# Optimization experiments

Hardware: AMD Instinct MI355X
Metric: run time of the kernel (lower is better)

## Reference

```python
import jax, jax.numpy as jnp
import numpy as np

N = 500_000   # active voxels
K = 27        # 3x3x3 kernel offsets
CIN = 32
COUT = 64
EPS = 1e-5


def setup_inputs() -> dict:
    key = jax.random.key(0)
    ks = jax.random.split(key, 9)
    x_feats = jax.random.normal(ks[0], (N, CIN), jnp.float32)
    # neighbor map: for each kernel offset k and output voxel i, index of the
    # input voxel contributing through offset k (submanifold conv, stride=1)
    nbr = jax.random.randint(ks[1], (K, N), 0, N, jnp.int32)
    s1 = 1.0 / np.sqrt(K * CIN)
    s2 = 1.0 / np.sqrt(K * COUT)
    w1 = jax.random.normal(ks[2], (K, CIN, COUT), jnp.float32) * s1
    w2 = jax.random.normal(ks[3], (K, COUT, COUT), jnp.float32) * s2
    g1 = jnp.ones((COUT,), jnp.float32)
    b1 = jnp.zeros((COUT,), jnp.float32)
    g2 = jnp.ones((COUT,), jnp.float32)
    b2 = jnp.zeros((COUT,), jnp.float32)
    wid = jax.random.normal(ks[4], (CIN, COUT), jnp.float32) * (1.0 / np.sqrt(CIN))
    gid = jnp.ones((COUT,), jnp.float32)
    bid = jnp.zeros((COUT,), jnp.float32)
    return {"x_feats": x_feats, "nbr": nbr, "w1": w1, "g1": g1, "b1": b1,
            "w2": w2, "g2": g2, "b2": b2, "wid": wid, "gid": gid, "bid": bid}


def _sparse_conv(feats, nbr, W):
    # feats [N, Cin], nbr [K, N], W [K, Cin, Cout]
    # scan over the fixed 27 kernel offsets: gather -> matmul -> accumulate
    def step(acc, kw):
        idx, w = kw
        return acc + feats[idx] @ w, None
    out0 = jnp.zeros((feats.shape[0], W.shape[-1]), feats.dtype)
    out, _ = jax.lax.scan(step, out0, (nbr, W))
    return out


def _bn(x, g, b):
    # training-mode BatchNorm1d over the voxel axis (biased variance, as torch)
    m = jnp.mean(x, axis=0)
    v = jnp.var(x, axis=0)
    return (x - m) * jax.lax.rsqrt(v + EPS) * g + b


def reference(x_feats, nbr, w1, g1, b1, w2, g2, b2, wid, gid, bid):
    h = jax.nn.relu(_bn(_sparse_conv(x_feats, nbr, w1), g1, b1))
    h = _bn(_sparse_conv(h, nbr, w2), g2, b2)
    ident = _bn(x_feats @ wid, gid, bid)
    return jax.nn.relu(h + ident)
```

## Files before the change

kernel.cpp:

```cpp
#include <hip/hip_runtime.h>

#define NV 500000
#define KOFF 27
#define CIN_ 32
#define COUT_ 64
#define EPS_ 1e-5f

typedef __attribute__((ext_vector_type(8))) _Float16 half8;
typedef __attribute__((ext_vector_type(4))) float floatx4;


__global__ void zero_stats_kernel(float* __restrict__ s) {
  if (threadIdx.x < 384) s[threadIdx.x] = 0.f;
}

__global__ __launch_bounds__(256) void cast_x_kernel(
    const float* __restrict__ x, _Float16* __restrict__ xh) {
  size_t q = (size_t)blockIdx.x * 256 + threadIdx.x;
  if (q >= (size_t)NV * CIN_ / 8) return;
  const float4* xp = (const float4*)x;
  float4 a = xp[2 * q], b = xp[2 * q + 1];
  half8 h;
  h[0] = (_Float16)a.x; h[1] = (_Float16)a.y; h[2] = (_Float16)a.z; h[3] = (_Float16)a.w;
  h[4] = (_Float16)b.x; h[5] = (_Float16)b.y; h[6] = (_Float16)b.z; h[7] = (_Float16)b.w;
  ((half8*)xh)[q] = h;
}

__global__ void wtrans_kernel(const float* __restrict__ w,
                              _Float16* __restrict__ wT, int CI) {
  int t = blockIdx.x * 256 + threadIdx.x;
  int total = KOFF * CI * COUT_;
  if (t >= total) return;
  int k = t / (CI * COUT_);
  int r = t % (CI * COUT_);
  int co = r / CI;
  int ci = r % CI;
  wT[t] = (_Float16)w[(k * CI + ci) * COUT_ + co];
}


template<int CI>
__device__ __forceinline__ void stageB_v6(const _Float16* __restrict__ wT,
                                          _Float16* __restrict__ lds,
                                          int k0, int kp, int tid) {
  __syncthreads();
  const int segs = CI / 8;
  const int chunks = kp * COUT_ * segs;
  for (int idx = tid; idx < chunks; idx += 256) {
    int row = idx / segs;
    int s = idx - row * segs;
    half8 v = *(const half8*)(wT + ((size_t)k0 * COUT_ + row) * CI + s * 8);
    *(half8*)(lds + (size_t)row * (CI + 8) + s * 8) = v;
  }
  __syncthreads();
}

template<int CI, int KPC, int D>
__device__ __forceinline__ void run_phase_v6(
    const half8* __restrict__ fp, const int* __restrict__ nbr,
    const _Float16* __restrict__ lds, int k0,
    int v0, int m, int quad, floatx4 acc[4]) {
  constexpr int SEG = CI / 32;
  constexpr int ROWH8 = CI / 8;

  int j0[KPC];
#pragma unroll
  for (int k = 0; k < KPC; ++k) j0[k] = nbr[(k0 + k) * NV + v0] * ROWH8;

  half8 ring[D][SEG];
#pragma unroll
  for (int p = 0; p < D; ++p)
#pragma unroll
    for (int s = 0; s < SEG; ++s)
      ring[p][s] = fp[(size_t)j0[p] + s * 4 + quad];

#pragma unroll
  for (int k = 0; k < KPC; ++k) {
    const _Float16* bk = lds + (size_t)k * COUT_ * (CI + 8);
#pragma unroll
    for (int s = 0; s < SEG; ++s)
#pragma unroll
      for (int nf = 0; nf < 4; ++nf) {
        half8 bf = *(const half8*)(bk + (nf * 16 + m) * (CI + 8) + s * 32 + quad * 8);
        acc[nf] = __builtin_amdgcn_mfma_f32_16x16x32_f16(ring[k % D][s], bf, acc[nf], 0, 0, 0);
      }
    if (k + D < KPC) {
#pragma unroll
      for (int s = 0; s < SEG; ++s)
        ring[k % D][s] = fp[(size_t)j0[k + D] + s * 4 + quad];
    }
  }
}

template<int CI, bool WF16>
__global__ __launch_bounds__(256, 5) void conv_mfma_v6(
    const _Float16* __restrict__ feats, const int* __restrict__ nbr,
    const _Float16* __restrict__ wT, float* __restrict__ outF,
    _Float16* __restrict__ outH, float* __restrict__ stOut) {
  constexpr int LDSH = 3 * 64 * (CI + 8);
  __shared__ __align__(16) _Float16 ldsB[LDSH];
  __shared__ float bs[128];

  int tid = threadIdx.x;
  int wave = tid >> 6, lane = tid & 63;
  int m = lane & 15, quad = lane >> 4;
  int vbase = (blockIdx.x * 4 + wave) * 16;
  int v0 = vbase + m;
  v0 = v0 < NV ? v0 : NV - 1;
  const half8* fp = (const half8*)feats;

  if (tid < 128) bs[tid] = 0.f;

  floatx4 acc[4];
#pragma unroll
  for (int nf = 0; nf < 4; ++nf) acc[nf] = (floatx4){0.f, 0.f, 0.f, 0.f};

#pragma unroll
  for (int ph = 0; ph < 9; ++ph) {
    stageB_v6<CI>(wT, ldsB, ph * 3, 3, tid);
    run_phase_v6<CI, 3, 3>(fp, nbr, ldsB, ph * 3, v0, m, quad, acc);
  }

  float s4[4], q4[4];
#pragma unroll
  for (int nf = 0; nf < 4; ++nf) {
    float s = 0.f, q = 0.f;
#pragma unroll
    for (int r = 0; r < 4; ++r) {
      int row = vbase + quad * 4 + r;
      if (row < NV) {
        float v = acc[nf][r];
        size_t o = (size_t)row * COUT_ + nf * 16 + m;
        if constexpr (WF16) outH[o] = (_Float16)v;
        else outF[o] = v;
        s += v;
        q = fmaf(v, v, q);
      }
    }
    s4[nf] = s; q4[nf] = q;
  }
#pragma unroll
  for (int nf = 0; nf < 4; ++nf) {
    s4[nf] += __shfl_xor(s4[nf], 16); s4[nf] += __shfl_xor(s4[nf], 32);
    q4[nf] += __shfl_xor(q4[nf], 16); q4[nf] += __shfl_xor(q4[nf], 32);
  }
  if (quad == 0) {
#pragma unroll
    for (int nf = 0; nf < 4; ++nf) {
      atomicAdd(&bs[nf * 16 + m], s4[nf]);
      atomicAdd(&bs[64 + nf * 16 + m], q4[nf]);
    }
  }
  __syncthreads();
  if (tid < 128) atomicAdd(&stOut[tid], bs[tid]);
}


__global__ __launch_bounds__(256) void ident_stats_kernel(
    const float* __restrict__ x, const float* __restrict__ wid,
    float* __restrict__ sums) {
  int lane = threadIdx.x & 63;
  int wv = blockIdx.x * 4 + (threadIdx.x >> 6);
  int nw = gridDim.x * 4;
  float wcol[CIN_];
#pragma unroll
  for (int ci = 0; ci < CIN_; ++ci) wcol[ci] = wid[ci * COUT_ + lane];
  float s = 0.f, ss = 0.f;
  for (int v = wv; v < NV; v += nw) {
    const float* xr = x + (size_t)v * CIN_;
    float d = 0.f;
#pragma unroll
    for (int ci = 0; ci < CIN_; ++ci) d = fmaf(xr[ci], wcol[ci], d);
    s += d;
    ss = fmaf(d, d, ss);
  }
  __shared__ float ls[128];
  if (threadIdx.x < 128) ls[threadIdx.x] = 0.f;
  __syncthreads();
  atomicAdd(&ls[lane], s);
  atomicAdd(&ls[64 + lane], ss);
  __syncthreads();
  if (threadIdx.x < 128) atomicAdd(&sums[threadIdx.x], ls[threadIdx.x]);
}

__global__ void finalize_kernel(const float* __restrict__ sums,
                                const float* __restrict__ g,
                                const float* __restrict__ b,
                                float* __restrict__ out) {
  int c = threadIdx.x;
  float m = sums[c] * (1.0f / NV);
  float var = sums[64 + c] * (1.0f / NV) - m * m;
  float sc = g[c] / sqrtf(var + EPS_);
  out[c] = sc;
  out[64 + c] = b[c] - m * sc;
}

__global__ __launch_bounds__(256) void bnrelu_f16_kernel(
    _Float16* __restrict__ y, const float* __restrict__ scsh) {
  size_t q = (size_t)blockIdx.x * 256 + threadIdx.x;
  if (q >= (size_t)NV * COUT_ / 8) return;
  int c0 = (int)(q & 7) * 8;
  half8 v = ((const half8*)y)[q];
#pragma unroll
  for (int jj = 0; jj < 8; ++jj) {
    float f = fmaxf(fmaf((float)v[jj], scsh[c0 + jj], scsh[64 + c0 + jj]), 0.f);
    v[jj] = (_Float16)f;
  }
  ((half8*)y)[q] = v;
}

__global__ __launch_bounds__(256) void final_kernel(
    const float* __restrict__ x, const float* __restrict__ wid,
    float* __restrict__ y2out, const float* __restrict__ ss2,
    const float* __restrict__ ssid) {
  int lane = threadIdx.x & 63;
  int wv = blockIdx.x * 4 + (threadIdx.x >> 6);
  int nw = gridDim.x * 4;
  float wcol[CIN_];
#pragma unroll
  for (int ci = 0; ci < CIN_; ++ci) wcol[ci] = wid[ci * COUT_ + lane];
  float sc2 = ss2[lane], sh2 = ss2[64 + lane];
  float sci = ssid[lane], shi = ssid[64 + lane];
  for (int v = wv; v < NV; v += nw) {
    const float* xr = x + (size_t)v * CIN_;
    float d = 0.f;
#pragma unroll
    for (int ci = 0; ci < CIN_; ++ci) d = fmaf(xr[ci], wcol[ci], d);
    size_t o = (size_t)v * COUT_ + lane;
    float r = fmaf(y2out[o], sc2, sh2) + fmaf(d, sci, shi);
    y2out[o] = fmaxf(r, 0.f);
  }
}

extern "C" void kernel_launch(void* const* d_in, const int* in_sizes, int n_in,
                              void* d_out, int out_size, void* d_ws, size_t ws_size,
                              hipStream_t stream) {
  const float* x   = (const float*)d_in[0];
  const int*   nbr = (const int*)d_in[1];
  const float* w1  = (const float*)d_in[2];
  const float* g1  = (const float*)d_in[3];
  const float* b1  = (const float*)d_in[4];
  const float* w2  = (const float*)d_in[5];
  const float* g2  = (const float*)d_in[6];
  const float* b2  = (const float*)d_in[7];
  const float* wid = (const float*)d_in[8];
  const float* gid = (const float*)d_in[9];
  const float* bid = (const float*)d_in[10];
  float* out = (float*)d_out;

  _Float16* y1h = (_Float16*)d_ws;
  _Float16* xh  = y1h + (size_t)NV * COUT_;
  _Float16* wT1 = xh + (size_t)NV * CIN_;
  _Float16* wT2 = wT1 + KOFF * COUT_ * CIN_;
  float*    st  = (float*)(wT2 + KOFF * COUT_ * COUT_);

  const int NWG = (NV + 63) / 64;

  zero_stats_kernel<<<1, 384, 0, stream>>>(st);
  cast_x_kernel<<<(NV * CIN_ / 8 + 255) / 256, 256, 0, stream>>>(x, xh);
  wtrans_kernel<<<(KOFF * CIN_ * COUT_ + 255) / 256, 256, 0, stream>>>(w1, wT1, CIN_);
  wtrans_kernel<<<(KOFF * COUT_ * COUT_ + 255) / 256, 256, 0, stream>>>(w2, wT2, COUT_);

  conv_mfma_v6<CIN_, true><<<NWG, 256, 0, stream>>>(xh, nbr, wT1, nullptr, y1h, st + 0);
  ident_stats_kernel<<<2048, 256, 0, stream>>>(x, wid, st + 256);
  finalize_kernel<<<1, 64, 0, stream>>>(st + 0, g1, b1, st + 384);
  finalize_kernel<<<1, 64, 0, stream>>>(st + 256, gid, bid, st + 640);
  bnrelu_f16_kernel<<<(NV * COUT_ / 8 + 255) / 256, 256, 0, stream>>>(y1h, st + 384);

  conv_mfma_v6<COUT_, false><<<NWG, 256, 0, stream>>>(y1h, nbr, wT2, out, nullptr, st + 128);
  finalize_kernel<<<1, 64, 0, stream>>>(st + 128, g2, b2, st + 512);
  final_kernel<<<4096, 256, 0, stream>>>(x, wid, out, st + 512, st + 640);
}
```

Measured before the change: 1.195 ms.

## Use 1024-thread conv blocks with full weight staging and deeper gather prefetch

Each conv workgroup grows from 4 to 16 waves. For the 32-channel conv, all 27 offset weight slices are staged into LDS once instead of nine separate 3-offset stages. For the 64-channel conv, staging happens in three 9-offset chunks. The gather prefetch ring is deepened to 7–8 offsets, aiming to cut barrier and restaging overhead and expose more memory-level parallelism. In exchange, LDS use per block rises sharply, which limits residency to roughly one block per CU. The deeper ring and the (1024,4) launch bound also raise register pressure and the risk of spills.

```diff
diff --git a/kernel.cpp b/kernel.cpp
--- a/kernel.cpp
+++ b/kernel.cpp
@@ -39,24 +39,24 @@
 }
 
 
-template<int CI>
-__device__ __forceinline__ void stageB_v6(const _Float16* __restrict__ wT,
+template<int CI, int PAD>
+__device__ __forceinline__ void stageB_v8(const _Float16* __restrict__ wT,
                                           _Float16* __restrict__ lds,
                                           int k0, int kp, int tid) {
   __syncthreads();
   const int segs = CI / 8;
   const int chunks = kp * COUT_ * segs;
-  for (int idx = tid; idx < chunks; idx += 256) {
+  for (int idx = tid; idx < chunks; idx += 1024) {
     int row = idx / segs;
     int s = idx - row * segs;
     half8 v = *(const half8*)(wT + ((size_t)k0 * COUT_ + row) * CI + s * 8);
-    *(half8*)(lds + (size_t)row * (CI + 8) + s * 8) = v;
-  }
-  __syncthreads();
-}
-
-template<int CI, int KPC, int D>
-__device__ __forceinline__ void run_phase_v6(
+    *(half8*)(lds + (size_t)row * (CI + PAD) + s * 8) = v;
+  }
+  __syncthreads();
+}
+
+template<int CI, int PAD, int KPC, int D>
+__device__ __forceinline__ void run_phase_v8(
     const half8* __restrict__ fp, const int* __restrict__ nbr,
     const _Float16* __restrict__ lds, int k0,
     int v0, int m, int quad, floatx4 acc[4]) {
@@ -76,12 +76,12 @@
 
 #pragma unroll
   for (int k = 0; k < KPC; ++k) {
-    const _Float16* bk = lds + (size_t)k * COUT_ * (CI + 8);
+    const _Float16* bk = lds + (size_t)k * COUT_ * (CI + PAD);
 #pragma unroll
     for (int s = 0; s < SEG; ++s)
 #pragma unroll
       for (int nf = 0; nf < 4; ++nf) {
-        half8 bf = *(const half8*)(bk + (nf * 16 + m) * (CI + 8) + s * 32 + quad * 8);
+        half8 bf = *(const half8*)(bk + (nf * 16 + m) * (CI + PAD) + s * 32 + quad * 8);
         acc[nf] = __builtin_amdgcn_mfma_f32_16x16x32_f16(ring[k % D][s], bf, acc[nf], 0, 0, 0);
       }
     if (k + D < KPC) {
@@ -93,18 +93,19 @@
 }
 
 template<int CI, bool WF16>
-__global__ __launch_bounds__(256, 5) void conv_mfma_v6(
+__global__ __launch_bounds__(1024, 4) void conv_mfma_v8(
     const _Float16* __restrict__ feats, const int* __restrict__ nbr,
     const _Float16* __restrict__ wT, float* __restrict__ outF,
     _Float16* __restrict__ outH, float* __restrict__ stOut) {
-  constexpr int LDSH = 3 * 64 * (CI + 8);
+  constexpr int PAD = 8;
+  constexpr int LDSH = (CI == 64) ? 9 * 64 * (64 + PAD) : 27 * 64 * (32 + PAD);
   __shared__ __align__(16) _Float16 ldsB[LDSH];
   __shared__ float bs[128];
 
   int tid = threadIdx.x;
   int wave = tid >> 6, lane = tid & 63;
   int m = lane & 15, quad = lane >> 4;
-  int vbase = (blockIdx.x * 4 + wave) * 16;
+  int vbase = (blockIdx.x * 16 + wave) * 16;
   int v0 = vbase + m;
   v0 = v0 < NV ? v0 : NV - 1;
   const half8* fp = (const half8*)feats;
@@ -115,10 +116,16 @@
 #pragma unroll
   for (int nf = 0; nf < 4; ++nf) acc[nf] = (floatx4){0.f, 0.f, 0.f, 0.f};
 
-#pragma unroll
-  for (int ph = 0; ph < 9; ++ph) {
-    stageB_v6<CI>(wT, ldsB, ph * 3, 3, tid);
-    run_phase_v6<CI, 3, 3>(fp, nbr, ldsB, ph * 3, v0, m, quad, acc);
+  if constexpr (CI == 64) {
+    stageB_v8<CI, PAD>(wT, ldsB, 0, 9, tid);
+    run_phase_v8<CI, PAD, 9, 7>(fp, nbr, ldsB, 0, v0, m, quad, acc);
+    stageB_v8<CI, PAD>(wT, ldsB, 9, 9, tid);
+    run_phase_v8<CI, PAD, 9, 7>(fp, nbr, ldsB, 9, v0, m, quad, acc);
+    stageB_v8<CI, PAD>(wT, ldsB, 18, 9, tid);
+    run_phase_v8<CI, PAD, 9, 7>(fp, nbr, ldsB, 18, v0, m, quad, acc);
+  } else {
+    stageB_v8<CI, PAD>(wT, ldsB, 0, 27, tid);
+    run_phase_v8<CI, PAD, 27, 8>(fp, nbr, ldsB, 0, v0, m, quad, acc);
   }
 
   float s4[4], q4[4];
@@ -254,20 +261,20 @@
   _Float16* wT2 = wT1 + KOFF * COUT_ * CIN_;
   float*    st  = (float*)(wT2 + KOFF * COUT_ * COUT_);
 
-  const int NWG = (NV + 63) / 64;
+  const int NWG = (NV + 255) / 256;
 
   zero_stats_kernel<<<1, 384, 0, stream>>>(st);
   cast_x_kernel<<<(NV * CIN_ / 8 + 255) / 256, 256, 0, stream>>>(x, xh);
   wtrans_kernel<<<(KOFF * CIN_ * COUT_ + 255) / 256, 256, 0, stream>>>(w1, wT1, CIN_);
   wtrans_kernel<<<(KOFF * COUT_ * COUT_ + 255) / 256, 256, 0, stream>>>(w2, wT2, COUT_);
 
-  conv_mfma_v6<CIN_, true><<<NWG, 256, 0, stream>>>(xh, nbr, wT1, nullptr, y1h, st + 0);
+  conv_mfma_v8<CIN_, true><<<NWG, 1024, 0, stream>>>(xh, nbr, wT1, nullptr, y1h, st + 0);
   ident_stats_kernel<<<2048, 256, 0, stream>>>(x, wid, st + 256);
   finalize_kernel<<<1, 64, 0, stream>>>(st + 0, g1, b1, st + 384);
   finalize_kernel<<<1, 64, 0, stream>>>(st + 256, gid, bid, st + 640);
   bnrelu_f16_kernel<<<(NV * COUT_ / 8 + 255) / 256, 256, 0, stream>>>(y1h, st + 384);
 
-  conv_mfma_v6<COUT_, false><<<NWG, 256, 0, stream>>>(y1h, nbr, wT2, out, nullptr, st + 128);
+  conv_mfma_v8<COUT_, false><<<NWG, 1024, 0, stream>>>(y1h, nbr, wT2, out, nullptr, st + 128);
   finalize_kernel<<<1, 64, 0, stream>>>(st + 128, g2, b2, st + 512);
   final_kernel<<<4096, 256, 0, stream>>>(x, wid, out, st + 512, st + 640);
 }
```

Result: slower. 3.203 ms (+168.1%).
